# Kernel tuning notes

Hardware: AMD Instinct MI355X
Metric: run time of the kernel (lower is better)

The kernel has to match this reference:

```python
import jax, jax.numpy as jnp
import numpy as np

B, H, N = 2, 4, 4096


def setup_inputs() -> dict:
    key = jax.random.key(0)
    ranking = jax.random.normal(key, (B, H, N, 1), dtype=jnp.float32)
    return {"ranking": ranking}


def reference(ranking):
    b_s, h, n = ranking.shape[:3]
    r = ranking[..., 0]  # [b, h, n]
    # stable descending argsort of ranking*100 (negate; jnp stable sort keeps tie order)
    sorted_idx = jnp.argsort(-r * 100.0, axis=2, stable=True)  # [b, h, n] int
    r_sort = jnp.take_along_axis(r, sorted_idx, axis=2)
    # rel_scaler = cumsum of ones = 1..n (no mask case)
    rel_scaler = jnp.cumsum(jnp.ones_like(r_sort), axis=2)
    rel_minus = jnp.cumsum(r_sort, axis=2)
    relative_ranking = rel_minus - rel_scaler * r_sort
    rel_scaler = jnp.maximum(rel_scaler - 1.0, 0.0)  # 0..n-1
    # Hrelu forward: hard ReLU (custom backward in torch; forward math is relu)
    rank = jax.nn.relu(relative_ranking)
    indicator = rel_scaler - rank
    indicator = jnp.where(indicator < 0, indicator + n, indicator)
    perm_value = jnp.exp(-indicator * 10.0)
    # sparse COO (bh, row, col) -> coalesce == scatter-add into dense [b*h, n, n]
    rows = rel_scaler.astype(jnp.int32).reshape(b_s * h, n)
    cols = sorted_idx.reshape(b_s * h, n).astype(jnp.int32)
    vals = perm_value.reshape(b_s * h, n)
    bh = jnp.arange(b_s * h, dtype=jnp.int32)[:, None]
    perm = jnp.zeros((b_s * h, n, n), jnp.float32).at[bh, rows, cols].add(vals)
    return perm
```

## Files before the change

kernel.cpp:

```cpp
#include <hip/hip_runtime.h>
#include <math.h>

#define N 4096
#define BH 8
#define THREADS 256
#define PARTS 32
#define EPB 128
#define EPT 4
#define SLICES 8
#define KPS (N / SLICES)
#define CHUNK (N / THREADS)
#define FILL_BLOCKS 4096
#define RPB (BH * N / FILL_BLOCKS)

__device__ __forceinline__ unsigned long long desc_key64(float r, int i) {
    float k = r * 100.0f;
    unsigned int b = __float_as_uint(k);
    unsigned int asc = (b & 0x80000000u) ? ~b : (b | 0x80000000u);
    return ((unsigned long long)(~asc) << 32) | (unsigned int)i;
}

__global__ __launch_bounds__(THREADS)
void rank_kernel(const float* __restrict__ ranking,
                 int* __restrict__ cols,
                 float* __restrict__ rsort) {
    __shared__ unsigned long long keys[N];
    __shared__ unsigned short partial[SLICES * EPB];

    const int bh   = blockIdx.x / PARTS;
    const int part = blockIdx.x % PARTS;
    const float* r = ranking + (size_t)bh * N;

    const float4* r4 = (const float4*)r;
    for (int i = threadIdx.x; i < N / 4; i += THREADS) {
        float4 w = r4[i];
        keys[i * 4 + 0] = desc_key64(w.x, i * 4 + 0);
        keys[i * 4 + 1] = desc_key64(w.y, i * 4 + 1);
        keys[i * 4 + 2] = desc_key64(w.z, i * 4 + 2);
        keys[i * 4 + 3] = desc_key64(w.w, i * 4 + 3);
    }
    __syncthreads();

    const int g = threadIdx.x & 31;
    const int s = threadIdx.x >> 5;
    const int e_base = g * EPT;

    unsigned long long mykey[EPT];
    #pragma unroll
    for (int j = 0; j < EPT; ++j)
        mykey[j] = keys[part * EPB + e_base + j];

    int cnt0 = 0, cnt1 = 0, cnt2 = 0, cnt3 = 0;
    const ulonglong2* k2 = (const ulonglong2*)(keys + s * KPS);
    #pragma unroll 4
    for (int k = 0; k < KPS / 2; ++k) {
        ulonglong2 kk = k2[k];
        cnt0 += (kk.x < mykey[0]) + (kk.y < mykey[0]);
        cnt1 += (kk.x < mykey[1]) + (kk.y < mykey[1]);
        cnt2 += (kk.x < mykey[2]) + (kk.y < mykey[2]);
        cnt3 += (kk.x < mykey[3]) + (kk.y < mykey[3]);
    }
    partial[s * EPB + e_base + 0] = (unsigned short)cnt0;
    partial[s * EPB + e_base + 1] = (unsigned short)cnt1;
    partial[s * EPB + e_base + 2] = (unsigned short)cnt2;
    partial[s * EPB + e_base + 3] = (unsigned short)cnt3;
    __syncthreads();

    if (threadIdx.x < EPB) {
        int rank = 0;
        #pragma unroll
        for (int t = 0; t < SLICES; ++t)
            rank += (int)partial[t * EPB + threadIdx.x];
        int e = part * EPB + threadIdx.x;
        size_t o = (size_t)bh * N + rank;
        cols[o]  = e;
        rsort[o] = r[e];
    }
}

__global__ __launch_bounds__(THREADS)
void scan_kernel(const float* __restrict__ rsort,
                 float* __restrict__ vals) {
    __shared__ double chunk_sums[THREADS];

    const int bh  = blockIdx.x;
    const int tid = threadIdx.x;
    const float* rs = rsort + (size_t)bh * N;
    const int base = tid * CHUNK;

    float  v[CHUNK];
    double local[CHUNK];
    const float4* f4 = (const float4*)(rs + base);
    #pragma unroll
    for (int q = 0; q < CHUNK / 4; ++q) {
        float4 w = f4[q];
        v[q * 4 + 0] = w.x; v[q * 4 + 1] = w.y;
        v[q * 4 + 2] = w.z; v[q * 4 + 3] = w.w;
    }
    double s = 0.0;
    #pragma unroll
    for (int q = 0; q < CHUNK; ++q) { s += (double)v[q]; local[q] = s; }
    chunk_sums[tid] = s;
    __syncthreads();

    double off = 0.0;
    for (int t = 0; t < tid; ++t) off += chunk_sums[t];

    #pragma unroll
    for (int q = 0; q < CHUNK; ++q) {
        int i = base + q;
        double cumsum = off + local[q];
        double rel    = cumsum - (double)(i + 1) * (double)v[q];
        double rank   = rel > 0.0 ? rel : 0.0;
        double ind    = (double)i - rank;
        if (ind < 0.0) ind += (double)N;
        if (ind < 0.0) ind = 0.0;
        vals[(size_t)bh * N + i] = (float)exp(ind * -10.0);
    }
}

__global__ __launch_bounds__(THREADS)
void fill_kernel(const int* __restrict__ cols,
                 const float* __restrict__ vals,
                 float* __restrict__ out) {
    const int tid = threadIdx.x;
    const size_t row0 = (size_t)blockIdx.x * RPB;

    int   c[RPB];
    float v[RPB];
    #pragma unroll
    for (int rr = 0; rr < RPB; ++rr) {
        c[rr] = cols[row0 + rr];
        v[rr] = vals[row0 + rr];
    }

    #pragma unroll
    for (int rr = 0; rr < RPB; ++rr) {
        float4* o = (float4*)(out + (row0 + rr) * (size_t)N);
        const int fc = c[rr] >> 2;
        #pragma unroll
        for (int q = 0; q < 4; ++q) {
            int f = tid + THREADS * q;
            float4 w = {0.f, 0.f, 0.f, 0.f};
            if (f == fc) ((float*)&w)[c[rr] & 3] = v[rr];
            o[f] = w;
        }
    }
}

extern "C" void kernel_launch(void* const* d_in, const int* in_sizes, int n_in,
                              void* d_out, int out_size, void* d_ws, size_t ws_size,
                              hipStream_t stream) {
    const float* ranking = (const float*)d_in[0];
    float* out = (float*)d_out;

    int*   cols  = (int*)d_ws;
    float* rsort = (float*)((char*)d_ws + sizeof(int)     * (size_t)BH * N);
    float* vals  = (float*)((char*)d_ws + sizeof(int) * 2 * (size_t)BH * N);

    rank_kernel<<<BH * PARTS, THREADS, 0, stream>>>(ranking, cols, rsort);
    scan_kernel<<<BH, THREADS, 0, stream>>>(rsort, vals);
    fill_kernel<<<FILL_BLOCKS, THREADS, 0, stream>>>(cols, vals, out);
}
```

Measured before the change: 547.5 us.

## Fuse scan into fill kernel with per-block prefix reduction and nontemporal stores

Merges the scan and fill kernels. Each fill block now recomputes the prefix-sum offset for its rows by reducing chunk sums over all threads of its batch-head, and one thread computes the exponent values for the block's rows. This removes a kernel launch, the low-parallelism 8-block scan with its serial offset loop, and the intermediate vals buffer. The output zero-fill now uses nontemporal stores. In exchange, every block redundantly reads the whole rsort row and runs a shared-memory tree reduction.

```diff
diff --git a/kernel.cpp b/kernel.cpp
--- a/kernel.cpp
+++ b/kernel.cpp
@@ -12,6 +12,9 @@
 #define CHUNK (N / THREADS)
 #define FILL_BLOCKS 4096
 #define RPB (BH * N / FILL_BLOCKS)
+#define BPR (N / RPB)
+
+typedef float f32x4 __attribute__((ext_vector_type(4)));
 
 __device__ __forceinline__ unsigned long long desc_key64(float r, int i) {
     float k = r * 100.0f;
@@ -79,15 +82,24 @@
 }
 
 __global__ __launch_bounds__(THREADS)
-void scan_kernel(const float* __restrict__ rsort,
-                 float* __restrict__ vals) {
-    __shared__ double chunk_sums[THREADS];
+void scanfill_kernel(const int* __restrict__ cols,
+                     const float* __restrict__ rsort,
+                     float* __restrict__ out) {
+    __shared__ double sdata[THREADS];
+    __shared__ float  vals_l[RPB];
 
-    const int bh  = blockIdx.x;
     const int tid = threadIdx.x;
+    const int bh  = blockIdx.x / BPR;
+    const int i0  = (blockIdx.x % BPR) * RPB;
+    const size_t row0 = (size_t)bh * N + i0;
+    const int t0  = i0 / CHUNK;
+
+    int c[RPB];
+    #pragma unroll
+    for (int rr = 0; rr < RPB; ++rr) c[rr] = cols[row0 + rr];
+
     const float* rs = rsort + (size_t)bh * N;
     const int base = tid * CHUNK;
-
     float  v[CHUNK];
     double local[CHUNK];
     const float4* f4 = (const float4*)(rs + base);
@@ -97,53 +109,46 @@
         v[q * 4 + 0] = w.x; v[q * 4 + 1] = w.y;
         v[q * 4 + 2] = w.z; v[q * 4 + 3] = w.w;
     }
-    double s = 0.0;
+    double ssum = 0.0;
     #pragma unroll
-    for (int q = 0; q < CHUNK; ++q) { s += (double)v[q]; local[q] = s; }
-    chunk_sums[tid] = s;
+    for (int q = 0; q < CHUNK; ++q) { ssum += (double)v[q]; local[q] = ssum; }
+
+    sdata[tid] = (tid < t0) ? ssum : 0.0;
     __syncthreads();
+    #pragma unroll
+    for (int s = THREADS / 2; s > 0; s >>= 1) {
+        if (tid < s) sdata[tid] += sdata[tid + s];
+        __syncthreads();
+    }
+    const double off = sdata[0];
 
-    double off = 0.0;
-    for (int t = 0; t < tid; ++t) off += chunk_sums[t];
-
-    #pragma unroll
-    for (int q = 0; q < CHUNK; ++q) {
-        int i = base + q;
-        double cumsum = off + local[q];
-        double rel    = cumsum - (double)(i + 1) * (double)v[q];
-        double rank   = rel > 0.0 ? rel : 0.0;
-        double ind    = (double)i - rank;
-        if (ind < 0.0) ind += (double)N;
-        if (ind < 0.0) ind = 0.0;
-        vals[(size_t)bh * N + i] = (float)exp(ind * -10.0);
+    if (tid == t0) {
+        #pragma unroll
+        for (int rr = 0; rr < RPB; ++rr) {
+            int i = i0 + rr;
+            int q = i - base;
+            double cumsum = off + local[q];
+            double rel    = cumsum - (double)(i + 1) * (double)v[q];
+            double rank   = rel > 0.0 ? rel : 0.0;
+            double ind    = (double)i - rank;
+            if (ind < 0.0) ind += (double)N;
+            if (ind < 0.0) ind = 0.0;
+            vals_l[rr] = (float)exp(ind * -10.0);
+        }
     }
-}
-
-__global__ __launch_bounds__(THREADS)
-void fill_kernel(const int* __restrict__ cols,
-                 const float* __restrict__ vals,
-                 float* __restrict__ out) {
-    const int tid = threadIdx.x;
-    const size_t row0 = (size_t)blockIdx.x * RPB;
-
-    int   c[RPB];
-    float v[RPB];
-    #pragma unroll
-    for (int rr = 0; rr < RPB; ++rr) {
-        c[rr] = cols[row0 + rr];
-        v[rr] = vals[row0 + rr];
-    }
+    __syncthreads();
 
     #pragma unroll
     for (int rr = 0; rr < RPB; ++rr) {
-        float4* o = (float4*)(out + (row0 + rr) * (size_t)N);
+        f32x4* o = (f32x4*)(out + (row0 + rr) * (size_t)N);
         const int fc = c[rr] >> 2;
+        const float vv = vals_l[rr];
         #pragma unroll
         for (int q = 0; q < 4; ++q) {
             int f = tid + THREADS * q;
-            float4 w = {0.f, 0.f, 0.f, 0.f};
-            if (f == fc) ((float*)&w)[c[rr] & 3] = v[rr];
-            o[f] = w;
+            f32x4 w = {0.f, 0.f, 0.f, 0.f};
+            if (f == fc) w[c[rr] & 3] = vv;
+            __builtin_nontemporal_store(w, o + f);
         }
     }
 }
@@ -155,10 +160,8 @@
     float* out = (float*)d_out;
 
     int*   cols  = (int*)d_ws;
-    float* rsort = (float*)((char*)d_ws + sizeof(int)     * (size_t)BH * N);
-    float* vals  = (float*)((char*)d_ws + sizeof(int) * 2 * (size_t)BH * N);
+    float* rsort = (float*)((char*)d_ws + sizeof(int) * (size_t)BH * N);
 
     rank_kernel<<<BH * PARTS, THREADS, 0, stream>>>(ranking, cols, rsort);
-    scan_kernel<<<BH, THREADS, 0, stream>>>(rsort, vals);
-    fill_kernel<<<FILL_BLOCKS, THREADS, 0, stream>>>(cols, vals, out);
+    scanfill_kernel<<<FILL_BLOCKS, THREADS, 0, stream>>>(cols, rsort, out);
 }
```

Result: no change. 537.3 us (-1.9%).
